# Kernel tuning notes

Hardware: AMD Instinct MI355X
Metric: run time of the kernel (lower is better)

Reference implementation:

```python
import jax, jax.numpy as jnp
import numpy as np

N_NODES = 100000
N_EDGES = 3200000
N_FEAT = 24
LAYERS = 6
VAL_SCALE = 0.01  # keep repeated SpMM numerically tame


def setup_inputs() -> dict:
    key = jax.random.key(0)
    k1, k2, k3, k4 = jax.random.split(key, 4)
    x = jax.random.normal(k1, (N_NODES, N_FEAT), dtype=jnp.float32)
    values = jax.random.normal(k2, (N_EDGES,), dtype=jnp.float32) * VAL_SCALE
    row_idx = jax.random.randint(k3, (N_EDGES,), 0, N_NODES, dtype=jnp.int64)
    col_idx = jax.random.randint(k4, (N_EDGES,), 0, N_NODES, dtype=jnp.int64)
    return {"x": x, "values": values, "row_idx": row_idx, "col_idx": col_idx}


def _spmm(values, row_idx, col_idx, x):
    # out[r] = sum_{e: row[e]==r} values[e] * x[col[e]]   (COO SpMM)
    msgs = values[:, None] * x[col_idx]  # [E, F] gather + scale
    return jax.ops.segment_sum(msgs, row_idx, num_segments=N_NODES)


def reference(x, values, row_idx, col_idx):
    # Faithful to AdultConnectome.forward: result = A^LAYERS @ x with fixed
    # COO sparsity (torch.sparse.mm applied layer_number times).
    result = x
    for _ in range(LAYERS):
        result = _spmm(values, row_idx, col_idx, result)
    return result
```

## Files before the change

### kernel.cpp

```cpp
#include <hip/hip_runtime.h>

#define N_NODES 100000
#define N_EDGES 3200000
#define N_FEAT 24
#define PADF4 8
#define BSHIFT 7
#define BROWS 128
#define NBUCK ((N_NODES + BROWS - 1) >> BSHIFT)
#define PTHREADS 512
#define EPT 8
#define TILE (PTHREADS * EPT)
#define NTILES ((N_EDGES + TILE - 1) / TILE)
#define CAP 4352
#define DMAX 256
#define NKEY (BROWS * 16)

__device__ __forceinline__ int wave_incl_scan(int v, int lane) {
    #pragma unroll
    for (int off = 1; off < 64; off <<= 1) {
        int n = __shfl_up(v, off, 64);
        if (lane >= off) v += n;
    }
    return v;
}
__device__ __forceinline__ int block_excl_scan256(int v, int tid, int* wsum) {
    int lane = tid & 63, wid = tid >> 6;
    int inc = wave_incl_scan(v, lane);
    if (lane == 63) wsum[wid] = inc;
    __syncthreads();
    int base = 0;
    #pragma unroll
    for (int w = 0; w < 3; ++w) base += (w < wid) ? wsum[w] : 0;
    return base + inc - v;
}
__device__ __forceinline__ int block_excl_scan512(int v, int tid, int* wsum) {
    int lane = tid & 63, wid = tid >> 6;
    int inc = wave_incl_scan(v, lane);
    if (lane == 63) wsum[wid] = inc;
    __syncthreads();
    int base = 0;
    #pragma unroll
    for (int w = 0; w < 7; ++w) base += (w < wid) ? wsum[w] : 0;
    return base + inc - v;
}

__global__ __launch_bounds__(256) void bhist_kernel(const int* __restrict__ row,
                                                    int* __restrict__ bcnt) {
    __shared__ int h[NBUCK];
    for (int i = threadIdx.x; i < NBUCK; i += 256) h[i] = 0;
    __syncthreads();
    int stride = gridDim.x * blockDim.x;
    for (int i = blockIdx.x * blockDim.x + threadIdx.x; i < N_EDGES; i += stride)
        atomicAdd(&h[row[i] >> BSHIFT], 1);
    __syncthreads();
    for (int i = threadIdx.x; i < NBUCK; i += 256) {
        int c = h[i];
        if (c) atomicAdd(&bcnt[i], c);
    }
}

__global__ __launch_bounds__(1024) void bscan_kernel(const int* __restrict__ bcnt,
                                                     int* __restrict__ bbase,
                                                     int* __restrict__ bcursor) {
    __shared__ int part[1024];
    int tid = threadIdx.x;
    int v = (tid < NBUCK) ? bcnt[tid] : 0;
    part[tid] = v;
    __syncthreads();
    for (int off = 1; off < 1024; off <<= 1) {
        int p = (tid >= off) ? part[tid - off] : 0;
        __syncthreads();
        part[tid] += p;
        __syncthreads();
    }
    int ex = (tid > 0) ? part[tid - 1] : 0;
    if (tid <= NBUCK) {
        bbase[tid] = ex;
        if (tid < NBUCK) bcursor[tid] = ex;
    }
}

__global__ __launch_bounds__(PTHREADS) void part_kernel(const int* __restrict__ row,
                                                        const int* __restrict__ col,
                                                        const float* __restrict__ val,
                                                        int* __restrict__ bcursor,
                                                        int2* __restrict__ epk) {
    __shared__ int h[NBUCK];
    __shared__ int lstart[NBUCK];
    __shared__ int delta[NBUCK];
    __shared__ int wsum[8];
    __shared__ int2 stage[TILE];
    __shared__ unsigned short bidx[TILE];
    const int tid = threadIdx.x;
    for (int i = tid; i < NBUCK; i += PTHREADS) h[i] = 0;
    __syncthreads();

    const int tbase = blockIdx.x * TILE;
    const int m = min(TILE, N_EDGES - tbase);
    const int base = tbase + tid * EPT;
    int rowj[EPT], rk[EPT];
    #pragma unroll
    for (int j = 0; j < EPT; ++j) {
        int e = base + j;
        if (e < N_EDGES) {
            int r = row[e];
            rowj[j] = r;
            rk[j] = atomicAdd(&h[r >> BSHIFT], 1);
        } else rowj[j] = -1;
    }
    __syncthreads();

    {
        int lo = tid * 2;
        int hi = min(NBUCK, lo + 2);
        int s = 0;
        for (int j = lo; j < hi; ++j) s += h[j];
        int run = block_excl_scan512(s, tid, wsum);
        for (int j = lo; j < hi; ++j) {
            lstart[j] = run;
            run += h[j];
        }
    }
    __syncthreads();

    for (int i = tid; i < NBUCK; i += PTHREADS) {
        int c = h[i];
        int g = c ? atomicAdd(&bcursor[i], c) : 0;
        delta[i] = g - lstart[i];
    }
    __syncthreads();

    #pragma unroll
    for (int j = 0; j < EPT; ++j) {
        if (rowj[j] >= 0) {
            int e = base + j;
            int b = rowj[j] >> BSHIFT;
            int rl = rowj[j] & (BROWS - 1);
            int slot = lstart[b] + rk[j];
            int2 pk;
            pk.x = col[e] | (rl << 17);
            pk.y = __float_as_int(val[e]);
            stage[slot] = pk;
            bidx[slot] = (unsigned short)b;
        }
    }
    __syncthreads();

    for (int i = tid; i < m; i += PTHREADS) {
        int b = bidx[i];
        epk[delta[b] + i] = stage[i];
    }
}

__global__ __launch_bounds__(256) void place_kernel(const int* __restrict__ bbase,
                                                    int2* __restrict__ epk,
                                                    int* __restrict__ starts,
                                                    int* __restrict__ dcnt) {
    __shared__ int kcnt[NKEY];
    __shared__ int kcur[NKEY];
    __shared__ int wsum[4];
    __shared__ int dh[DMAX];
    __shared__ int2 stage[CAP];
    int b = blockIdx.x;
    int tid = threadIdx.x;
    int gb = bbase[b];
    int n = bbase[b + 1] - gb;
    for (int j = tid; j < NKEY; j += 256) kcnt[j] = 0;
    dh[tid] = 0;
    __syncthreads();
    for (int i = tid; i < n; i += 256) {
        int x = epk[gb + i].x;
        int key = (((x >> 17) & (BROWS - 1)) << 4) | ((x >> 13) & 15);
        atomicAdd(&kcnt[key], 1);
    }
    __syncthreads();
    int deg = 0;
    if (tid < BROWS) {
        int lo = tid << 4;
        #pragma unroll
        for (int j = 0; j < 16; ++j) deg += kcnt[lo + j];
    }
    int r_glob = (b << BSHIFT) + tid;
    if (tid < BROWS && r_glob < N_NODES) atomicAdd(&dh[min(deg, DMAX - 1)], 1);
    int run = block_excl_scan256(deg, tid, wsum);
    if (tid < BROWS && r_glob < N_NODES) starts[r_glob] = gb + run;
    if (b == 0 && tid == 0) starts[N_NODES] = N_EDGES;
    if (tid < BROWS) {
        int lo = tid << 4;
        #pragma unroll
        for (int j = 0; j < 16; ++j) {
            kcur[lo + j] = run;
            run += kcnt[lo + j];
        }
    }
    __syncthreads();
    {
        int c = dh[tid];
        if (c) atomicAdd(&dcnt[tid], c);
    }
    for (int i = tid; i < n; i += 256) {
        int2 p = epk[gb + i];
        int key = (((p.x >> 17) & (BROWS - 1)) << 4) | ((p.x >> 13) & 15);
        int slot = atomicAdd(&kcur[key], 1);
        int2 fin;
        fin.x = p.x & 0x1FFFF;
        fin.y = p.y;
        if (slot < CAP) stage[slot] = fin;
        else epk[gb + slot] = fin;
    }
    __syncthreads();
    for (int i = tid; i < n && i < CAP; i += 256) epk[gb + i] = stage[i];
}

__global__ __launch_bounds__(256) void dscan_kernel(const int* __restrict__ dcnt,
                                                    int* __restrict__ dcur) {
    __shared__ int part[DMAX];
    int tid = threadIdx.x;
    int v = dcnt[tid];
    part[tid] = v;
    __syncthreads();
    for (int off = 1; off < DMAX; off <<= 1) {
        int p = (tid >= off) ? part[tid - off] : 0;
        __syncthreads();
        part[tid] += p;
        __syncthreads();
    }
    dcur[tid] = N_NODES - part[tid];
}

__global__ __launch_bounds__(256) void dscatter_kernel(const int* __restrict__ starts,
                                                       int* __restrict__ dcur,
                                                       int* __restrict__ perm) {
    __shared__ int h[DMAX];
    __shared__ int chunk[DMAX];
    int tid = threadIdx.x;
    int r = blockIdx.x * 256 + tid;
    h[tid] = 0;
    __syncthreads();
    int d = -1, rk = 0;
    if (r < N_NODES) {
        d = min(starts[r + 1] - starts[r], DMAX - 1);
        rk = atomicAdd(&h[d], 1);
    }
    __syncthreads();
    int c = h[tid];
    chunk[tid] = c ? atomicAdd(&dcur[tid], c) : 0;
    __syncthreads();
    if (r < N_NODES) perm[chunk[d] + rk] = r;
}

__global__ __launch_bounds__(256) void pad_copy_kernel(const float4* __restrict__ x4,
                                                       float4* __restrict__ dst) {
    int t = blockIdx.x * blockDim.x + threadIdx.x;
    int r = t >> 3;
    if (r >= N_NODES) return;
    int sub = t & 7;
    float4 v;
    if (sub < 6) v = x4[r * 6 + sub];
    else         v = make_float4(0.f, 0.f, 0.f, 0.f);
    dst[r * PADF4 + sub] = v;
}

#define ACC4(v, xv, a)                                       \
    a.x = fmaf(v, xv.x, a.x); a.y = fmaf(v, xv.y, a.y);      \
    a.z = fmaf(v, xv.z, a.z); a.w = fmaf(v, xv.w, a.w);

__global__ __launch_bounds__(256) void spmm_pad_kernel(const int* __restrict__ starts,
                                                       const int* __restrict__ perm,
                                                       const int2* __restrict__ epk,
                                                       const float4* __restrict__ src,
                                                       float4* __restrict__ dst) {
    int t = blockIdx.x * blockDim.x + threadIdx.x;
    int g = t >> 3;
    if (g >= N_NODES) return;
    int rowi = perm[g];
    int sub = t & 7;
    int s = starts[rowi];
    int e = starts[rowi + 1];
    const float4* sp = src + sub;
    float4 acc = make_float4(0.f, 0.f, 0.f, 0.f);
    int i = s;
    for (; i + 3 < e; i += 4) {
        int2 p0 = epk[i];
        int2 p1 = epk[i + 1];
        int2 p2 = epk[i + 2];
        int2 p3 = epk[i + 3];
        float4 x0 = sp[p0.x * PADF4];
        float4 x1 = sp[p1.x * PADF4];
        float4 x2 = sp[p2.x * PADF4];
        float4 x3 = sp[p3.x * PADF4];
        ACC4(__int_as_float(p0.y), x0, acc);
        ACC4(__int_as_float(p1.y), x1, acc);
        ACC4(__int_as_float(p2.y), x2, acc);
        ACC4(__int_as_float(p3.y), x3, acc);
    }
    for (; i < e; ++i) {
        int2 p = epk[i];
        float4 xv = sp[p.x * PADF4];
        ACC4(__int_as_float(p.y), xv, acc);
    }
    dst[rowi * PADF4 + sub] = acc;
}

__global__ __launch_bounds__(256) void spmm_final_kernel(const int* __restrict__ starts,
                                                         const int* __restrict__ perm,
                                                         const int2* __restrict__ epk,
                                                         const float4* __restrict__ src,
                                                         float* __restrict__ out) {
    int t = blockIdx.x * blockDim.x + threadIdx.x;
    int g = t >> 3;
    if (g >= N_NODES) return;
    int rowi = perm[g];
    int sub = t & 7;
    int s = starts[rowi];
    int e = starts[rowi + 1];
    const float4* sp = src + sub;
    float4 acc = make_float4(0.f, 0.f, 0.f, 0.f);
    int i = s;
    for (; i + 3 < e; i += 4) {
        int2 p0 = epk[i];
        int2 p1 = epk[i + 1];
        int2 p2 = epk[i + 2];
        int2 p3 = epk[i + 3];
        float4 x0 = sp[p0.x * PADF4];
        float4 x1 = sp[p1.x * PADF4];
        float4 x2 = sp[p2.x * PADF4];
        float4 x3 = sp[p3.x * PADF4];
        ACC4(__int_as_float(p0.y), x0, acc);
        ACC4(__int_as_float(p1.y), x1, acc);
        ACC4(__int_as_float(p2.y), x2, acc);
        ACC4(__int_as_float(p3.y), x3, acc);
    }
    for (; i < e; ++i) {
        int2 p = epk[i];
        float4 xv = sp[p.x * PADF4];
        ACC4(__int_as_float(p.y), xv, acc);
    }
    if (sub < 6) *(float4*)(out + rowi * N_FEAT + sub * 4) = acc;
}


extern "C" void kernel_launch(void* const* d_in, const int* in_sizes, int n_in,
                              void* d_out, int out_size, void* d_ws, size_t ws_size,
                              hipStream_t stream) {
    const float* x       = (const float*)d_in[0];
    const float* values  = (const float*)d_in[1];
    const int*   row_idx = (const int*)d_in[2];
    const int*   col_idx = (const int*)d_in[3];
    float* out = (float*)d_out;

    char* ws = (char*)d_ws;
    int*    bcnt    = (int*)(ws + 0);
    int*    bbase   = (int*)(ws + 4096);
    int*    bcursor = (int*)(ws + 8192);
    int*    dcnt    = (int*)(ws + 12288);
    int*    dcur    = (int*)(ws + 16384);
    int*    starts  = (int*)(ws + 20480);
    int*    perm    = (int*)(ws + 420608);
    int2*   epk     = (int2*)(ws + 820736);
    float4* bufA    = (float4*)(ws + 26420864);
    float4* bufB    = (float4*)(ws + 39220864);

    hipMemsetAsync(bcnt, 0, NBUCK * sizeof(int), stream);
    hipMemsetAsync(dcnt, 0, DMAX * sizeof(int), stream);
    bhist_kernel<<<512, 256, 0, stream>>>(row_idx, bcnt);
    bscan_kernel<<<1, 1024, 0, stream>>>(bcnt, bbase, bcursor);
    part_kernel<<<NTILES, PTHREADS, 0, stream>>>(row_idx, col_idx, values, bcursor, epk);
    place_kernel<<<NBUCK, 256, 0, stream>>>(bbase, epk, starts, dcnt);

    const int node_blocks = (N_NODES + 255) / 256;
    dscan_kernel<<<1, DMAX, 0, stream>>>(dcnt, dcur);
    dscatter_kernel<<<node_blocks, 256, 0, stream>>>(starts, dcur, perm);

    const int spmm_blocks = (N_NODES * 8 + 255) / 256;
    pad_copy_kernel<<<spmm_blocks, 256, 0, stream>>>((const float4*)x, bufA);
    spmm_pad_kernel<<<spmm_blocks, 256, 0, stream>>>(starts, perm, epk, bufA, bufB);
    spmm_pad_kernel<<<spmm_blocks, 256, 0, stream>>>(starts, perm, epk, bufB, bufA);
    spmm_pad_kernel<<<spmm_blocks, 256, 0, stream>>>(starts, perm, epk, bufA, bufB);
    spmm_pad_kernel<<<spmm_blocks, 256, 0, stream>>>(starts, perm, epk, bufB, bufA);
    spmm_pad_kernel<<<spmm_blocks, 256, 0, stream>>>(starts, perm, epk, bufA, bufB);
    spmm_final_kernel<<<spmm_blocks, 256, 0, stream>>>(starts, perm, epk, bufB, out);
}
```

Before: 416.4 us.

## Vectorize histogram loads, widen partition blocks, use nontemporal edge loads in SpMM

The bucket histogram kernel now reads row indices as int4, four per load, which cuts load instructions. The partition kernel goes from 512 to 768 threads per block, with the block scan and the shared wsum array widened to match. Both SpMM kernels fetch packed edge entries with nontemporal loads so the streamed edge list does not evict the gathered feature rows from cache. A larger partition block raises shared-memory use per block, which may lower occupancy, and the nontemporal hint could hurt if edge data was being reused across the six layers.

```diff
diff --git a/kernel.cpp b/kernel.cpp
--- a/kernel.cpp
+++ b/kernel.cpp
@@ -7,7 +7,7 @@
 #define BSHIFT 7
 #define BROWS 128
 #define NBUCK ((N_NODES + BROWS - 1) >> BSHIFT)
-#define PTHREADS 512
+#define PTHREADS 768
 #define EPT 8
 #define TILE (PTHREADS * EPT)
 #define NTILES ((N_EDGES + TILE - 1) / TILE)
@@ -33,25 +33,31 @@
     for (int w = 0; w < 3; ++w) base += (w < wid) ? wsum[w] : 0;
     return base + inc - v;
 }
-__device__ __forceinline__ int block_excl_scan512(int v, int tid, int* wsum) {
+__device__ __forceinline__ int block_excl_scan768(int v, int tid, int* wsum) {
     int lane = tid & 63, wid = tid >> 6;
     int inc = wave_incl_scan(v, lane);
     if (lane == 63) wsum[wid] = inc;
     __syncthreads();
     int base = 0;
     #pragma unroll
-    for (int w = 0; w < 7; ++w) base += (w < wid) ? wsum[w] : 0;
+    for (int w = 0; w < 11; ++w) base += (w < wid) ? wsum[w] : 0;
     return base + inc - v;
 }
 
-__global__ __launch_bounds__(256) void bhist_kernel(const int* __restrict__ row,
+__global__ __launch_bounds__(256) void bhist_kernel(const int4* __restrict__ row4,
                                                     int* __restrict__ bcnt) {
     __shared__ int h[NBUCK];
     for (int i = threadIdx.x; i < NBUCK; i += 256) h[i] = 0;
     __syncthreads();
     int stride = gridDim.x * blockDim.x;
-    for (int i = blockIdx.x * blockDim.x + threadIdx.x; i < N_EDGES; i += stride)
-        atomicAdd(&h[row[i] >> BSHIFT], 1);
+    const int n4 = N_EDGES / 4;
+    for (int i = blockIdx.x * blockDim.x + threadIdx.x; i < n4; i += stride) {
+        int4 r = row4[i];
+        atomicAdd(&h[r.x >> BSHIFT], 1);
+        atomicAdd(&h[r.y >> BSHIFT], 1);
+        atomicAdd(&h[r.z >> BSHIFT], 1);
+        atomicAdd(&h[r.w >> BSHIFT], 1);
+    }
     __syncthreads();
     for (int i = threadIdx.x; i < NBUCK; i += 256) {
         int c = h[i];
@@ -88,7 +94,7 @@
     __shared__ int h[NBUCK];
     __shared__ int lstart[NBUCK];
     __shared__ int delta[NBUCK];
-    __shared__ int wsum[8];
+    __shared__ int wsum[12];
     __shared__ int2 stage[TILE];
     __shared__ unsigned short bidx[TILE];
     const int tid = threadIdx.x;
@@ -115,7 +121,7 @@
         int hi = min(NBUCK, lo + 2);
         int s = 0;
         for (int j = lo; j < hi; ++j) s += h[j];
-        int run = block_excl_scan512(s, tid, wsum);
+        int run = block_excl_scan768(s, tid, wsum);
         for (int j = lo; j < hi; ++j) {
             lstart[j] = run;
             run += h[j];
@@ -264,6 +270,14 @@
 #define ACC4(v, xv, a)                                       \
     a.x = fmaf(v, xv.x, a.x); a.y = fmaf(v, xv.y, a.y);      \
     a.z = fmaf(v, xv.z, a.z); a.w = fmaf(v, xv.w, a.w);
+
+__device__ __forceinline__ int2 nt_load_e(const int2* p) {
+    long long v = __builtin_nontemporal_load((const long long*)p);
+    int2 r;
+    r.x = (int)(v & 0xFFFFFFFFll);
+    r.y = (int)(v >> 32);
+    return r;
+}
 
 __global__ __launch_bounds__(256) void spmm_pad_kernel(const int* __restrict__ starts,
                                                        const int* __restrict__ perm,
@@ -281,10 +295,10 @@
     float4 acc = make_float4(0.f, 0.f, 0.f, 0.f);
     int i = s;
     for (; i + 3 < e; i += 4) {
-        int2 p0 = epk[i];
-        int2 p1 = epk[i + 1];
-        int2 p2 = epk[i + 2];
-        int2 p3 = epk[i + 3];
+        int2 p0 = nt_load_e(&epk[i]);
+        int2 p1 = nt_load_e(&epk[i + 1]);
+        int2 p2 = nt_load_e(&epk[i + 2]);
+        int2 p3 = nt_load_e(&epk[i + 3]);
         float4 x0 = sp[p0.x * PADF4];
         float4 x1 = sp[p1.x * PADF4];
         float4 x2 = sp[p2.x * PADF4];
@@ -318,10 +332,10 @@
     float4 acc = make_float4(0.f, 0.f, 0.f, 0.f);
     int i = s;
     for (; i + 3 < e; i += 4) {
-        int2 p0 = epk[i];
-        int2 p1 = epk[i + 1];
-        int2 p2 = epk[i + 2];
-        int2 p3 = epk[i + 3];
+        int2 p0 = nt_load_e(&epk[i]);
+        int2 p1 = nt_load_e(&epk[i + 1]);
+        int2 p2 = nt_load_e(&epk[i + 2]);
+        int2 p3 = nt_load_e(&epk[i + 3]);
         float4 x0 = sp[p0.x * PADF4];
         float4 x1 = sp[p1.x * PADF4];
         float4 x2 = sp[p2.x * PADF4];
@@ -363,7 +377,7 @@
 
     hipMemsetAsync(bcnt, 0, NBUCK * sizeof(int), stream);
     hipMemsetAsync(dcnt, 0, DMAX * sizeof(int), stream);
-    bhist_kernel<<<512, 256, 0, stream>>>(row_idx, bcnt);
+    bhist_kernel<<<512, 256, 0, stream>>>((const int4*)row_idx, bcnt);
     bscan_kernel<<<1, 1024, 0, stream>>>(bcnt, bbase, bcursor);
     part_kernel<<<NTILES, PTHREADS, 0, stream>>>(row_idx, col_idx, values, bcursor, epk);
     place_kernel<<<NBUCK, 256, 0, stream>>>(bbase, epk, starts, dcnt);
```

New measurement: 484.6 us. +16.4%, slower.
